# Optimization experiments

Hardware: AMD Instinct MI355X
Metric: run time of the kernel (lower is better)

Reference implementation:

```python
import jax, jax.numpy as jnp
import numpy as np
import math

HEAD_DIM = 64
HEAD_NUM = 8  # hidden_dim(512) // head_dim(64)
EPS = 1e-8


def modulated_linear(x, s, weight, aff_w, aff_b):
    # x: [B, N, IN], s: [B, S], weight: [OUT, IN], aff_w: [IN, S], aff_b: [IN]
    style = s @ aff_w.T + aff_b                       # [B, IN]
    w = weight[None, :, :] * style[:, None, :]        # [B, OUT, IN]
    demod = jax.lax.rsqrt(jnp.sum(w * w, axis=2) + EPS)  # [B, OUT]
    w = w * demod[:, :, None]
    return jnp.einsum('bni,boi->bno', x, w)           # [B, N, OUT]


def setup_inputs() -> dict:
    key = jax.random.key(0)
    ks = jax.random.split(key, 8)
    B, N, F, S = 8, 1024, 512, 512
    sc = 1.0 / math.sqrt(F)
    return {
        'x': jax.random.normal(ks[0], (B, N, F), dtype=jnp.float32),
        's': jax.random.normal(ks[1], (B, S), dtype=jnp.float32),
        'k_weight': jax.random.normal(ks[2], (F, F), dtype=jnp.float32) * sc,
        'k_aff_w': jax.random.normal(ks[3], (F, S), dtype=jnp.float32) * sc,
        'k_aff_b': jnp.ones((F,), dtype=jnp.float32),
        'o_weight': jax.random.normal(ks[4], (F, F), dtype=jnp.float32) * sc,
        'o_aff_w': jax.random.normal(ks[5], (F, S), dtype=jnp.float32) * sc,
        'o_aff_b': jnp.ones((F,), dtype=jnp.float32),
    }


def reference(x, s, k_weight, k_aff_w, k_aff_b, o_weight, o_aff_w, o_aff_b):
    B, N, _ = x.shape
    # Original code computes q, k, v all via k_mapping (faithful to the bug).
    kqv = modulated_linear(x, s, k_weight, k_aff_w, k_aff_b)  # [B, N, hidden]
    kqv = kqv.reshape(B, N, HEAD_NUM, HEAD_DIM)               # [B, N, H, D]
    q = k = v = kqv
    scale = 1.0 / math.sqrt(HEAD_DIM)
    scores = jnp.einsum('bnhd,bmhd->bhnm', q, k) * scale      # [B, H, N, N]
    attn = jax.nn.softmax(scores, axis=-1)
    out = jnp.einsum('bhnm,bmhd->bnhd', attn, v)              # [B, N, H, D]
    out = out.reshape(B, N, HEAD_NUM * HEAD_DIM)
    return modulated_linear(out, s, o_weight, o_aff_w, o_aff_b)
```

## Files before the change

### kernel.cpp

```cpp
#include <hip/hip_runtime.h>
#include <stdint.h>

using short8  = __attribute__((ext_vector_type(8))) short;
using f32x4   = __attribute__((ext_vector_type(4))) float;
using float4v = __attribute__((ext_vector_type(4))) float;
using u16x4   = __attribute__((ext_vector_type(4))) unsigned short;

__device__ __forceinline__ unsigned short f2b(float f) {
    union { float f; unsigned int i; } v; v.f = f;
    unsigned int i = v.i;
    unsigned int r = (i + 0x7fffu + ((i >> 16) & 1u)) >> 16;
    return (unsigned short)r;
}
__device__ __forceinline__ unsigned short f2bt(float f) {
    union { float f; unsigned int i; } v; v.f = f;
    return (unsigned short)(v.i >> 16);
}
__device__ __forceinline__ short8 ld8(const unsigned short* p) {
    return *reinterpret_cast<const short8*>(p);
}
__device__ __forceinline__ void st8(unsigned short* p, short8 v) {
    *reinterpret_cast<short8*>(p) = v;
}
__device__ __forceinline__ f32x4 mfma16(short8 a, short8 b, f32x4 c) {
    return __builtin_amdgcn_mfma_f32_16x16x32_bf16(a, b, c, 0, 0, 0);
}
__device__ __forceinline__ void stC(float* p, float v)          { *p = v; }
__device__ __forceinline__ void stC(unsigned short* p, float v) { *p = f2b(v); }

__global__ __launch_bounds__(256) void cvt_kernel(const float* __restrict__ in,
                                                  unsigned short* __restrict__ out)
{
    int i = blockIdx.x * 256 + threadIdx.x;
    float4v v = reinterpret_cast<const float4v*>(in)[i];
    u16x4 o;
#pragma unroll
    for (int j = 0; j < 4; ++j) o[j] = f2b(v[j]);
    reinterpret_cast<u16x4*>(out)[i] = o;
}

__global__ __launch_bounds__(256) void style_kernel(
    const float* __restrict__ s,
    const float* __restrict__ k_aff_w, const float* __restrict__ k_aff_b,
    const float* __restrict__ o_aff_w, const float* __restrict__ o_aff_b,
    float* __restrict__ style)
{
    int wid  = blockIdx.x * 4 + (threadIdx.x >> 6);
    int lane = threadIdx.x & 63;
    int map  = wid >> 12;
    int rem  = wid & 4095;
    int b    = rem >> 9;
    int i    = rem & 511;
    const float* aw = map ? o_aff_w : k_aff_w;
    const float* ab = map ? o_aff_b : k_aff_b;
    const float* sp = s  + b * 512 + lane * 8;
    const float* wp = aw + i * 512 + lane * 8;
    float acc = 0.f;
#pragma unroll
    for (int j = 0; j < 8; ++j) acc += sp[j] * wp[j];
#pragma unroll
    for (int off = 1; off < 64; off <<= 1) acc += __shfl_xor(acc, off, 64);
    if (lane == 0) style[(map * 8 + b) * 512 + i] = acc + ab[i];
}

__global__ __launch_bounds__(256) void modw_kernel(
    const float* __restrict__ k_weight,
    const float* __restrict__ o_weight,
    const float* __restrict__ style,
    unsigned short* __restrict__ wmod)
{
    int wid  = blockIdx.x * 4 + (threadIdx.x >> 6);
    int lane = threadIdx.x & 63;
    int map  = wid >> 12;
    int rem  = wid & 4095;
    int b    = rem >> 9;
    int o    = rem & 511;
    const float* wrow = (map ? o_weight : k_weight) + o * 512 + lane * 8;
    const float* st   = style + (map * 8 + b) * 512 + lane * 8;
    float w[8]; float ss = 0.f;
#pragma unroll
    for (int j = 0; j < 8; ++j) { w[j] = wrow[j] * st[j]; ss += w[j] * w[j]; }
#pragma unroll
    for (int off = 1; off < 64; off <<= 1) ss += __shfl_xor(ss, off, 64);
    float demod = rsqrtf(ss + 1e-8f);
    short8 ov;
#pragma unroll
    for (int j = 0; j < 8; ++j) ov[j] = (short)f2b(w[j] * demod);
    unsigned short* dst = wmod + (((size_t)map * 8 + b) * 512 + o) * 512 + lane * 8;
    *reinterpret_cast<short8*>(dst) = ov;
}

template <typename CT, bool WVT>
__global__ __launch_bounds__(256) void gemm_bt_lds_kernel(
    const unsigned short* __restrict__ A,
    const unsigned short* __restrict__ Bt,
    CT* __restrict__ C,
    unsigned short* __restrict__ VT)
{
    constexpr int KP = 72;
    constexpr int TP = 72;
    __shared__ __align__(16) unsigned short smem[4 * 64 * KP];
    typedef unsigned short Plane[64][KP];
    Plane* As = reinterpret_cast<Plane*>(smem);
    Plane* Bs = reinterpret_cast<Plane*>(smem + 2 * 64 * KP);

    int blk = blockIdx.x;
    int b   = blk & 7;
    int rem = blk >> 3;
    int mt  = rem & 15;
    int nt  = rem >> 4;
    int tid  = threadIdx.x;
    int w    = tid >> 6;
    int lane = tid & 63;
    int quad = lane >> 4;
    int r    = lane & 15;
    int wm   = w >> 1;
    int wn   = w & 1;

    const unsigned short* Ab = A  + ((size_t)b * 1024 + mt * 64) * 512;
    const unsigned short* Bb = Bt + ((size_t)b * 512  + nt * 64) * 512;

    int srow = tid >> 2;
    int scol = (tid & 3) * 8;
    const unsigned short* ga = Ab + (size_t)srow * 512 + scol;
    const unsigned short* gb = Bb + (size_t)srow * 512 + scol;

    f32x4 acc[2][2];
#pragma unroll
    for (int i = 0; i < 2; ++i)
#pragma unroll
        for (int j = 0; j < 2; ++j) acc[i][j] = f32x4{0.f, 0.f, 0.f, 0.f};

    short8 rg[2][4];

    st8(&As[0][srow][scol],      ld8(ga));
    st8(&As[0][srow][scol + 32], ld8(ga + 32));
    st8(&Bs[0][srow][scol],      ld8(gb));
    st8(&Bs[0][srow][scol + 32], ld8(gb + 32));
    rg[1][0] = ld8(ga + 64);  rg[1][1] = ld8(ga + 96);
    rg[1][2] = ld8(gb + 64);  rg[1][3] = ld8(gb + 96);
    __syncthreads();

#pragma unroll
    for (int ks = 0; ks < 8; ++ks) {
        int s = ks & 1;
        if (ks < 6) {
            int ko = (ks + 2) * 64;
            rg[s][0] = ld8(ga + ko);       rg[s][1] = ld8(ga + ko + 32);
            rg[s][2] = ld8(gb + ko);       rg[s][3] = ld8(gb + ko + 32);
        }
#pragma unroll
        for (int kh = 0; kh < 2; ++kh) {
            short8 af[2], bf[2];
#pragma unroll
            for (int i = 0; i < 2; ++i)
                af[i] = ld8(&As[s][wm * 32 + i * 16 + r][kh * 32 + quad * 8]);
#pragma unroll
            for (int j = 0; j < 2; ++j)
                bf[j] = ld8(&Bs[s][wn * 32 + j * 16 + r][kh * 32 + quad * 8]);
#pragma unroll
            for (int i = 0; i < 2; ++i)
#pragma unroll
                for (int j = 0; j < 2; ++j)
                    acc[i][j] = mfma16(af[i], bf[j], acc[i][j]);
        }
        if (ks < 7) {
            int ns = s ^ 1;
            st8(&As[ns][srow][scol],      rg[ns][0]);
            st8(&As[ns][srow][scol + 32], rg[ns][1]);
            st8(&Bs[ns][srow][scol],      rg[ns][2]);
            st8(&Bs[ns][srow][scol + 32], rg[ns][3]);
        }
        __syncthreads();
    }

    CT* Cb = C + (size_t)b * 1024 * 512;
#pragma unroll
    for (int i = 0; i < 2; ++i)
#pragma unroll
        for (int rr = 0; rr < 4; ++rr) {
            int row = mt * 64 + wm * 32 + i * 16 + quad * 4 + rr;
#pragma unroll
            for (int j = 0; j < 2; ++j) {
                int col = nt * 64 + wn * 32 + j * 16 + r;
                stC(Cb + (size_t)row * 512 + col, acc[i][j][rr]);
            }
        }
    if (WVT) {
        unsigned short (*Tt)[TP] = reinterpret_cast<unsigned short (*)[TP]>(smem);
#pragma unroll
        for (int i = 0; i < 2; ++i)
#pragma unroll
            for (int j = 0; j < 2; ++j) {
                int d = wn * 32 + j * 16 + r;
#pragma unroll
                for (int rh = 0; rh < 2; ++rh) {
                    int tok = wm * 32 + i * 16 + quad * 4 + rh * 2;
                    unsigned int pv = (unsigned int)f2b(acc[i][j][rh * 2]) |
                                      ((unsigned int)f2b(acc[i][j][rh * 2 + 1]) << 16);
                    *reinterpret_cast<unsigned int*>(&Tt[d][tok]) = pv;
                }
            }
        __syncthreads();
        int d  = tid >> 2;
        int cc = tid & 3;
        const unsigned short* src = &Tt[d][cc * 16];
        unsigned short* dst = VT + ((size_t)(b * 8 + nt) * 64 + d) * 1024 + mt * 64 + cc * 16;
        short8 t0 = ld8(src), t1 = ld8(src + 8);
        st8(dst,     t0);
        st8(dst + 8, t1);
    }
}

__global__ __launch_bounds__(256) void attn_kernel(
    const unsigned short* __restrict__ kqv,
    const unsigned short* __restrict__ vt,
    unsigned short* __restrict__ attn_out)
{
    constexpr int PAD = 72;
    int blk = blockIdx.x;
    int bh = blk & 63;
    int qt = blk >> 6;
    int b  = bh >> 3, h = bh & 7;
    int tid  = threadIdx.x;
    int wv   = tid >> 6;
    int lane = tid & 63;
    int quad = lane >> 4;
    int r    = lane & 15;

    __shared__ __align__(16) unsigned short klds[2][64][PAD];
    __shared__ __align__(16) unsigned short vlds[2][64][PAD];
    __shared__ __align__(16) unsigned short plds[4][16][PAD];
    unsigned short* myp = &plds[wv][0][0];

    const unsigned short* Mb = kqv + (size_t)b * 1024 * 512;
    int q0 = qt * 64 + wv * 16;

    const unsigned short* qptr = Mb + (size_t)(q0 + r) * 512 + h * 64 + quad * 8;
    short8 bq0 = ld8(qptr);
    short8 bq1 = ld8(qptr + 32);

    short8 ones;
#pragma unroll
    for (int j = 0; j < 8; ++j) ones[j] = (short)0x3F80;

    f32x4 o0 = {0.f, 0.f, 0.f, 0.f};
    f32x4 o1 = o0, o2 = o0, o3 = o0, lacc = o0;

    int srow0 = tid >> 3;
    int srow1 = srow0 + 32;
    int scol  = (tid & 7) * 8;
    const unsigned short* Kg = Mb + h * 64;
    const unsigned short* Vg = vt + (size_t)bh * 64 * 1024;

    {
        short8 k0v = ld8(Kg + (size_t)srow0 * 512 + scol);
        short8 k1v = ld8(Kg + (size_t)srow1 * 512 + scol);
        short8 v0v = ld8(Vg + (size_t)srow0 * 1024 + scol);
        short8 v1v = ld8(Vg + (size_t)srow1 * 1024 + scol);
        st8(&klds[0][srow0][scol], k0v);
        st8(&klds[0][srow1][scol], k1v);
        st8(&vlds[0][srow0][scol], v0v);
        st8(&vlds[0][srow1][scol], v1v);
    }
    __syncthreads();

    const float c  = 0.18033688011112042f;
    const float CM = 28.853900817779268f;

    for (int it = 0; it < 16; ++it) {
        int s = it & 1;
        short8 pk0, pk1, pv0, pv1;
        if (it < 15) {
            int k0n = (it + 1) * 64;
            pk0 = ld8(Kg + (size_t)(k0n + srow0) * 512 + scol);
            pk1 = ld8(Kg + (size_t)(k0n + srow1) * 512 + scol);
            pv0 = ld8(Vg + (size_t)srow0 * 1024 + k0n + scol);
            pv1 = ld8(Vg + (size_t)srow1 * 1024 + k0n + scol);
        }
        f32x4 st_[4];
#pragma unroll
        for (int t = 0; t < 4; ++t) {
            short8 ka = ld8(&klds[s][t * 16 + r][quad * 8]);
            short8 kb = ld8(&klds[s][t * 16 + r][32 + quad * 8]);
            f32x4 sacc = {0.f, 0.f, 0.f, 0.f};
            sacc = mfma16(ka, bq0, sacc);
            sacc = mfma16(kb, bq1, sacc);
            st_[t] = sacc;
        }
#pragma unroll
        for (int t = 0; t < 4; ++t) {
            u16x4 pb;
#pragma unroll
            for (int rr = 0; rr < 4; ++rr)
                pb[rr] = f2bt(exp2f(st_[t][rr] * c - CM));
            *reinterpret_cast<u16x4*>(&myp[r * PAD + t * 16 + quad * 4]) = pb;
        }
        short8 ap0 = ld8(&myp[r * PAD + quad * 8]);
        short8 ap1 = ld8(&myp[r * PAD + 32 + quad * 8]);
        {
            short8 va, vb;
            va = ld8(&vlds[s][0 * 16 + r][quad * 8]);
            vb = ld8(&vlds[s][0 * 16 + r][32 + quad * 8]);
            o0 = mfma16(ap0, va, o0);  o0 = mfma16(ap1, vb, o0);
            va = ld8(&vlds[s][1 * 16 + r][quad * 8]);
            vb = ld8(&vlds[s][1 * 16 + r][32 + quad * 8]);
            o1 = mfma16(ap0, va, o1);  o1 = mfma16(ap1, vb, o1);
            va = ld8(&vlds[s][2 * 16 + r][quad * 8]);
            vb = ld8(&vlds[s][2 * 16 + r][32 + quad * 8]);
            o2 = mfma16(ap0, va, o2);  o2 = mfma16(ap1, vb, o2);
            va = ld8(&vlds[s][3 * 16 + r][quad * 8]);
            vb = ld8(&vlds[s][3 * 16 + r][32 + quad * 8]);
            o3 = mfma16(ap0, va, o3);  o3 = mfma16(ap1, vb, o3);
            lacc = mfma16(ap0, ones, lacc);
            lacc = mfma16(ap1, ones, lacc);
        }
        if (it < 15) {
            int ns = s ^ 1;
            st8(&klds[ns][srow0][scol], pk0);
            st8(&klds[ns][srow1][scol], pk1);
            st8(&vlds[ns][srow0][scol], pv0);
            st8(&vlds[ns][srow1][scol], pv1);
        }
        __syncthreads();
    }

    unsigned short* ob = attn_out + (size_t)b * 1024 * 512 + (size_t)h * 64;
#pragma unroll
    for (int rr = 0; rr < 4; ++rr) {
        float inv = 1.0f / lacc[rr];
        int n = q0 + quad * 4 + rr;
        unsigned short* orow = ob + (size_t)n * 512 + r;
        orow[0]  = f2b(o0[rr] * inv);
        orow[16] = f2b(o1[rr] * inv);
        orow[32] = f2b(o2[rr] * inv);
        orow[48] = f2b(o3[rr] * inv);
    }
}

extern "C" void kernel_launch(void* const* d_in, const int* in_sizes, int n_in,
                              void* d_out, int out_size, void* d_ws, size_t ws_size,
                              hipStream_t stream)
{
    const float* x        = (const float*)d_in[0];
    const float* s        = (const float*)d_in[1];
    const float* k_weight = (const float*)d_in[2];
    const float* k_aff_w  = (const float*)d_in[3];
    const float* k_aff_b  = (const float*)d_in[4];
    const float* o_weight = (const float*)d_in[5];
    const float* o_aff_w  = (const float*)d_in[6];
    const float* o_aff_b  = (const float*)d_in[7];
    float* out = (float*)d_out;

    char* ws = (char*)d_ws;
    float* style          = (float*)ws;
    unsigned short* wmod  = (unsigned short*)(ws + 32 * 1024);
    unsigned short* xbf   = wmod + (size_t)2 * 8 * 512 * 512;
    unsigned short* kqv   = xbf  + (size_t)8 * 1024 * 512;
    unsigned short* vt    = kqv  + (size_t)8 * 1024 * 512;
    unsigned short* attn  = xbf;

    cvt_kernel<<<4096, 256, 0, stream>>>(x, xbf);
    style_kernel<<<2048, 256, 0, stream>>>(s, k_aff_w, k_aff_b, o_aff_w, o_aff_b, style);
    modw_kernel<<<2048, 256, 0, stream>>>(k_weight, o_weight, style, wmod);
    gemm_bt_lds_kernel<unsigned short, true><<<1024, 256, 0, stream>>>(xbf, wmod, kqv, vt);
    attn_kernel<<<1024, 256, 0, stream>>>(kqv, vt, attn);
    gemm_bt_lds_kernel<float, false><<<1024, 256, 0, stream>>>(attn, wmod + (size_t)8 * 512 * 512, out, nullptr);
}
```

Measured before the change: 155.0 us.

## Load full-K tiles into LDS once instead of double-buffered K pipeline

The two projection GEMMs now stage the whole 64x512 A and B tiles into dynamic shared memory in one upfront pass, then run all 16 MFMA k-steps without per-step barriers. This removes the register-staged double buffer and the eight __syncthreads in the K loop. In exchange each block uses about 133KB of LDS, which limits occupancy to roughly one block per CU and gives up overlap of global loads with compute. A barrier is added before the transpose epilogue reuses shared memory.

```diff
diff --git a/kernel.cpp b/kernel.cpp
--- a/kernel.cpp
+++ b/kernel.cpp
@@ -91,18 +91,17 @@
 }
 
 template <typename CT, bool WVT>
-__global__ __launch_bounds__(256) void gemm_bt_lds_kernel(
+__global__ __launch_bounds__(256) void gemm_fullk_kernel(
     const unsigned short* __restrict__ A,
     const unsigned short* __restrict__ Bt,
     CT* __restrict__ C,
     unsigned short* __restrict__ VT)
 {
-    constexpr int KP = 72;
+    constexpr int KP = 520;
     constexpr int TP = 72;
-    __shared__ __align__(16) unsigned short smem[4 * 64 * KP];
-    typedef unsigned short Plane[64][KP];
-    Plane* As = reinterpret_cast<Plane*>(smem);
-    Plane* Bs = reinterpret_cast<Plane*>(smem + 2 * 64 * KP);
+    extern __shared__ __align__(16) unsigned short smem[];
+    unsigned short (*As)[KP] = reinterpret_cast<unsigned short (*)[KP]>(smem);
+    unsigned short (*Bs)[KP] = reinterpret_cast<unsigned short (*)[KP]>(smem + 64 * KP);
 
     int blk = blockIdx.x;
     int b   = blk & 7;
@@ -121,9 +120,24 @@
     const unsigned short* Bb = Bt + ((size_t)b * 512  + nt * 64) * 512;
 
     int srow = tid >> 2;
-    int scol = (tid & 3) * 8;
-    const unsigned short* ga = Ab + (size_t)srow * 512 + scol;
-    const unsigned short* gb = Bb + (size_t)srow * 512 + scol;
+    int sc0  = (tid & 3) * 8;
+    const unsigned short* ga = Ab + (size_t)srow * 512 + sc0;
+    const unsigned short* gb = Bb + (size_t)srow * 512 + sc0;
+    unsigned short* la = &As[srow][sc0];
+    unsigned short* lb = &Bs[srow][sc0];
+#pragma unroll
+    for (int half = 0; half < 2; ++half) {
+        short8 t[8];
+#pragma unroll
+        for (int j = 0; j < 8; ++j) t[j] = ld8(ga + (half * 8 + j) * 32);
+#pragma unroll
+        for (int j = 0; j < 8; ++j) st8(la + (half * 8 + j) * 32, t[j]);
+#pragma unroll
+        for (int j = 0; j < 8; ++j) t[j] = ld8(gb + (half * 8 + j) * 32);
+#pragma unroll
+        for (int j = 0; j < 8; ++j) st8(lb + (half * 8 + j) * 32, t[j]);
+    }
+    __syncthreads();
 
     f32x4 acc[2][2];
 #pragma unroll
@@ -131,47 +145,20 @@
 #pragma unroll
         for (int j = 0; j < 2; ++j) acc[i][j] = f32x4{0.f, 0.f, 0.f, 0.f};
 
-    short8 rg[2][4];
-
-    st8(&As[0][srow][scol],      ld8(ga));
-    st8(&As[0][srow][scol + 32], ld8(ga + 32));
-    st8(&Bs[0][srow][scol],      ld8(gb));
-    st8(&Bs[0][srow][scol + 32], ld8(gb + 32));
-    rg[1][0] = ld8(ga + 64);  rg[1][1] = ld8(ga + 96);
-    rg[1][2] = ld8(gb + 64);  rg[1][3] = ld8(gb + 96);
-    __syncthreads();
-
-#pragma unroll
-    for (int ks = 0; ks < 8; ++ks) {
-        int s = ks & 1;
-        if (ks < 6) {
-            int ko = (ks + 2) * 64;
-            rg[s][0] = ld8(ga + ko);       rg[s][1] = ld8(ga + ko + 32);
-            rg[s][2] = ld8(gb + ko);       rg[s][3] = ld8(gb + ko + 32);
-        }
-#pragma unroll
-        for (int kh = 0; kh < 2; ++kh) {
-            short8 af[2], bf[2];
-#pragma unroll
-            for (int i = 0; i < 2; ++i)
-                af[i] = ld8(&As[s][wm * 32 + i * 16 + r][kh * 32 + quad * 8]);
-#pragma unroll
-            for (int j = 0; j < 2; ++j)
-                bf[j] = ld8(&Bs[s][wn * 32 + j * 16 + r][kh * 32 + quad * 8]);
-#pragma unroll
-            for (int i = 0; i < 2; ++i)
-#pragma unroll
-                for (int j = 0; j < 2; ++j)
-                    acc[i][j] = mfma16(af[i], bf[j], acc[i][j]);
-        }
-        if (ks < 7) {
-            int ns = s ^ 1;
-            st8(&As[ns][srow][scol],      rg[ns][0]);
-            st8(&As[ns][srow][scol + 32], rg[ns][1]);
-            st8(&Bs[ns][srow][scol],      rg[ns][2]);
-            st8(&Bs[ns][srow][scol + 32], rg[ns][3]);
-        }
-        __syncthreads();
+    const unsigned short* a0 = &As[wm * 32 + r][quad * 8];
+    const unsigned short* a1 = &As[wm * 32 + 16 + r][quad * 8];
+    const unsigned short* b0 = &Bs[wn * 32 + r][quad * 8];
+    const unsigned short* b1 = &Bs[wn * 32 + 16 + r][quad * 8];
+#pragma unroll
+    for (int ks = 0; ks < 16; ++ks) {
+        short8 af0 = ld8(a0 + ks * 32);
+        short8 af1 = ld8(a1 + ks * 32);
+        short8 bf0 = ld8(b0 + ks * 32);
+        short8 bf1 = ld8(b1 + ks * 32);
+        acc[0][0] = mfma16(af0, bf0, acc[0][0]);
+        acc[0][1] = mfma16(af0, bf1, acc[0][1]);
+        acc[1][0] = mfma16(af1, bf0, acc[1][0]);
+        acc[1][1] = mfma16(af1, bf1, acc[1][1]);
     }
 
     CT* Cb = C + (size_t)b * 1024 * 512;
@@ -187,6 +174,7 @@
             }
         }
     if (WVT) {
+        __syncthreads();
         unsigned short (*Tt)[TP] = reinterpret_cast<unsigned short (*)[TP]>(smem);
 #pragma unroll
         for (int i = 0; i < 2; ++i)
@@ -360,10 +348,16 @@
     unsigned short* vt    = kqv  + (size_t)8 * 1024 * 512;
     unsigned short* attn  = xbf;
 
+    constexpr int GEMM_LDS = 2 * 64 * 520 * 2;
+    (void)hipFuncSetAttribute((const void*)gemm_fullk_kernel<unsigned short, true>,
+                              hipFuncAttributeMaxDynamicSharedMemorySize, GEMM_LDS);
+    (void)hipFuncSetAttribute((const void*)gemm_fullk_kernel<float, false>,
+                              hipFuncAttributeMaxDynamicSharedMemorySize, GEMM_LDS);
+
     cvt_kernel<<<4096, 256, 0, stream>>>(x, xbf);
     style_kernel<<<2048, 256, 0, stream>>>(s, k_aff_w, k_aff_b, o_aff_w, o_aff_b, style);
     modw_kernel<<<2048, 256, 0, stream>>>(k_weight, o_weight, style, wmod);
-    gemm_bt_lds_kernel<unsigned short, true><<<1024, 256, 0, stream>>>(xbf, wmod, kqv, vt);
+    gemm_fullk_kernel<unsigned short, true><<<1024, 256, GEMM_LDS, stream>>>(xbf, wmod, kqv, vt);
     attn_kernel<<<1024, 256, 0, stream>>>(kqv, vt, attn);
-    gemm_bt_lds_kernel<float, false><<<1024, 256, 0, stream>>>(attn, wmod + (size_t)8 * 512 * 512, out, nullptr);
-}
+    gemm_fullk_kernel<float, false><<<1024, 256, GEMM_LDS, stream>>>(attn, wmod + (size_t)8 * 512 * 512, out, nullptr);
+}
```

Result: slower. 161.0 us (+3.8%).
